# Kernel tuning notes

Hardware: AMD Instinct MI355X
Metric: run time of the kernel (lower is better)

The kernel has to match this reference:

```python
import jax, jax.numpy as jnp
import numpy as np

NUM_HEADS = 8
KEY_DIM = 16
D_V = 32  # attn_ratio * key_dim


def _conv1x1_bn(x, w, s, b):
    # x: [B, Cin, H, W], w: [Cout, Cin]; 1x1 conv == channel contraction,
    # eval-mode BatchNorm folded into per-channel scale s and bias b.
    y = jnp.einsum('bchw,oc->bohw', x, w)
    return y * s[:, None, None] + b[:, None, None]


def setup_inputs() -> dict:
    key = jax.random.key(0)
    ks = jax.random.split(key, 14)
    B, C, H, W = 16, 256, 32, 32
    nh_kd, dh = NUM_HEADS * KEY_DIM, NUM_HEADS * D_V
    f = jax.random.normal
    return {
        'x': f(ks[0], (B, C, H, W), jnp.float32),
        'wq': f(ks[1], (nh_kd, C), jnp.float32) * 0.05,
        'sq': jax.random.uniform(ks[2], (nh_kd,), jnp.float32),
        'bq': f(ks[3], (nh_kd,), jnp.float32) * 0.05,
        'wk': f(ks[4], (nh_kd, C), jnp.float32) * 0.05,
        'sk': jax.random.uniform(ks[5], (nh_kd,), jnp.float32),
        'bk': f(ks[6], (nh_kd,), jnp.float32) * 0.05,
        'wv': f(ks[7], (dh, C), jnp.float32) * 0.05,
        'sv': jax.random.uniform(ks[8], (dh,), jnp.float32),
        'bv': f(ks[9], (dh,), jnp.float32) * 0.05,
        'wp': f(ks[10], (C, dh), jnp.float32) * 0.05,
        'sp': jax.random.uniform(ks[11], (C,), jnp.float32),
        'bp': f(ks[12], (C,), jnp.float32) * 0.05,
    }


def reference(x, wq, sq, bq, wk, sk, bk, wv, sv, bv, wp, sp, bp):
    B, C, H, W = x.shape
    N = H * W
    # QKV projections (1x1 conv + folded BN)
    q = _conv1x1_bn(x, wq, sq, bq).reshape(B, NUM_HEADS, KEY_DIM, N)  # b h k n
    k = _conv1x1_bn(x, wk, sk, bk).reshape(B, NUM_HEADS, KEY_DIM, N)  # b h k m
    v = _conv1x1_bn(x, wv, sv, bv).reshape(B, NUM_HEADS, D_V, N)      # b h d m
    # NOTE: the original forward does NOT apply self.scale to the scores.
    attn = jnp.einsum('bhkn,bhkm->bhnm', q, k)
    attn = jax.nn.softmax(attn, axis=-1)
    out = jnp.einsum('bhnm,bhdm->bhdn', attn, v)  # b h d n
    out = out.reshape(B, NUM_HEADS * D_V, H, W)
    # proj = Sequential(activation, Conv2d_BN): activation FIRST
    out = jax.nn.relu(out)
    return _conv1x1_bn(out, wp, sp, bp)
```

## Files before the change

kernel.cpp:

```cpp
#include <hip/hip_runtime.h>

#define NTOT 1024
#define CIN  256
#define BATCH 16
#define NH   8
#define KD   16
#define DV   32
#define L2E  1.44269504088896340736f

typedef unsigned short u16;
typedef unsigned int   u32;
typedef __attribute__((ext_vector_type(2)))  _Float16 f16x2;
typedef __attribute__((ext_vector_type(8)))  _Float16 f16x8;
typedef __attribute__((ext_vector_type(16))) float    f32x16;

__device__ inline f16x8 as_f16x8(uint4 u) { return __builtin_bit_cast(f16x8, u); }
__device__ inline f16x2 as_f16x2(u32 u)   { return __builtin_bit_cast(f16x2, u); }
__device__ inline u32 pkrtz(float a, float b) {
  return __builtin_bit_cast(u32, __builtin_amdgcn_cvt_pkrtz(a, b));
}
__device__ inline u16 f2h(float x) {
  return __builtin_bit_cast(u16, (_Float16)x);
}
__device__ inline float fexp2(float x) {
#if __has_builtin(__builtin_amdgcn_exp2f)
  return __builtin_amdgcn_exp2f(x);
#else
  float r; asm("v_exp_f32 %0, %1" : "=v"(r) : "v"(x)); return r;
#endif
}
__device__ inline float dot2acc(u32 p2, float c) {
#if __has_builtin(__builtin_amdgcn_fdot2)
  const f16x2 one2 = __builtin_bit_cast(f16x2, (u32)0x3C003C00u);
  return __builtin_amdgcn_fdot2(as_f16x2(p2), one2, c, false);
#else
  const f16x2 v = as_f16x2(p2);
  return c + (float)v[0] + (float)v[1];
#endif
}

__global__ __launch_bounds__(256) void prep_fused(
    const float* __restrict__ X, u16* __restrict__ Xt,
    const float* __restrict__ wq, const float* __restrict__ sq, const float* __restrict__ bq,
    const float* __restrict__ wk, const float* __restrict__ sk, const float* __restrict__ bk,
    const float* __restrict__ wv, const float* __restrict__ sv, const float* __restrict__ bv,
    const float* __restrict__ wp, const float* __restrict__ sp, const float* __restrict__ bp,
    u16* __restrict__ wqkv, u16* __restrict__ wph, float* __restrict__ ball)
{
  __shared__ u16 T[64][64];
  const int bx = blockIdx.x;
  const int t  = threadIdx.x;
  if (bx < 1024) {
    const int n0 = (bx & 15) * 64;
    const int c0 = ((bx >> 4) & 3) * 64;
    const int b  = bx >> 6;
    #pragma unroll
    for (int rr = 0; rr < 4; ++rr) {
      const int c  = rr*16 + (t>>4);
      const int n4 = (t&15)*4;
      const float4 v = *(const float4*)&X[((size_t)b*CIN + c0 + c)*NTOT + n0 + n4];
      ushort4 r; r.x=f2h(v.x); r.y=f2h(v.y); r.z=f2h(v.z); r.w=f2h(v.w);
      *(ushort4*)&T[c][n4] = r;
    }
    __syncthreads();
    const int nl = t & 63;
    #pragma unroll
    for (int j = 0; j < 2; ++j) {
      const int oct = (t>>6)*2 + j;
      uint4 w;
      w.x = (u32)T[oct*8+0][nl] | ((u32)T[oct*8+1][nl] << 16);
      w.y = (u32)T[oct*8+2][nl] | ((u32)T[oct*8+3][nl] << 16);
      w.z = (u32)T[oct*8+4][nl] | ((u32)T[oct*8+5][nl] << 16);
      w.w = (u32)T[oct*8+6][nl] | ((u32)T[oct*8+7][nl] << 16);
      *(uint4*)&Xt[((size_t)b*NTOT + n0 + nl)*CIN + c0 + oct*8] = w;
    }
  } else {
    const int row = (bx - 1024)*4 + (t>>6);
    const int ln  = t & 63;
    const float* src; u16* dst; float sc, bi;
    if (row < 128)      { src = wq + (size_t)row*CIN;       sc = sq[row]*L2E;     bi = bq[row]*L2E;     dst = wqkv + (size_t)row*CIN; }
    else if (row < 256) { src = wk + (size_t)(row-128)*CIN; sc = sk[row-128];     bi = bk[row-128];     dst = wqkv + (size_t)row*CIN; }
    else if (row < 512) { src = wv + (size_t)(row-256)*CIN; sc = sv[row-256];     bi = bv[row-256];     dst = wqkv + (size_t)row*CIN; }
    else                { src = wp + (size_t)(row-512)*CIN; sc = sp[row-512];     bi = bp[row-512];     dst = wph + (size_t)(row-512)*CIN; }
    const float4 v = *(const float4*)&src[ln*4];
    ushort4 r;
    r.x = f2h(v.x*sc); r.y = f2h(v.y*sc); r.z = f2h(v.z*sc); r.w = f2h(v.w*sc);
    *(ushort4*)&dst[ln*4] = r;
    if (ln == 0) ball[row] = bi;
  }
}

template<int BN, int MODE>
__global__ __launch_bounds__(256) void conv_mfma(
    const u16* __restrict__ Wh, const u16* __restrict__ Bt,
    const float* __restrict__ ball,
    u16* __restrict__ q_t, u16* __restrict__ k_t, u16* __restrict__ v_h,
    float* __restrict__ outp)
{
  constexpr int FN = BN / 64;
  constexpr int NB = BN / 32;
  __shared__ u16 A_lds[2][128 * 64];
  __shared__ u16 B_lds[2][BN * 64];
  const int t    = threadIdx.x;
  const int lane = t & 63;
  const int w    = t >> 6;
  const int wm = w >> 1, wn = w & 1;
  const int g = lane >> 5, nl = lane & 31;
  const int n0 = blockIdx.x * BN;
  const int m0 = blockIdx.y * 128;
  const int b  = blockIdx.z;

  f32x16 acc[2][FN] = {};
  uint4 rA[4], rB[NB];

  #pragma unroll
  for (int r = 0; r < 4; ++r) {
    const int idx = t + r*256, row = idx >> 3, ch = idx & 7;
    rA[r] = *(const uint4*)&Wh[(size_t)(m0+row)*CIN + ch*8];
  }
  #pragma unroll
  for (int r = 0; r < NB; ++r) {
    const int idx = t + r*256, row = idx >> 3, ch = idx & 7;
    rB[r] = *(const uint4*)&Bt[((size_t)b*NTOT + n0 + row)*CIN + ch*8];
  }
  #pragma unroll
  for (int r = 0; r < 4; ++r) {
    const int idx = t + r*256, row = idx >> 3, ch = idx & 7;
    *(uint4*)&A_lds[0][row*64 + ((ch ^ (row&7))*8)] = rA[r];
  }
  #pragma unroll
  for (int r = 0; r < NB; ++r) {
    const int idx = t + r*256, row = idx >> 3, ch = idx & 7;
    *(uint4*)&B_lds[0][row*64 + ((ch ^ (row&7))*8)] = rB[r];
  }
  __syncthreads();

  for (int it = 0; it < 4; ++it) {
    const int cur = it & 1;
    if (it < 3) {
      const int c0 = (it+1)*64;
      #pragma unroll
      for (int r = 0; r < 4; ++r) {
        const int idx = t + r*256, row = idx >> 3, ch = idx & 7;
        rA[r] = *(const uint4*)&Wh[(size_t)(m0+row)*CIN + c0 + ch*8];
      }
      #pragma unroll
      for (int r = 0; r < NB; ++r) {
        const int idx = t + r*256, row = idx >> 3, ch = idx & 7;
        rB[r] = *(const uint4*)&Bt[((size_t)b*NTOT + n0 + row)*CIN + c0 + ch*8];
      }
    }
    #pragma unroll
    for (int ks = 0; ks < 4; ++ks) {
      const int ch = 2*ks + g;
      f16x8 a[2], bb[FN];
      #pragma unroll
      for (int fi = 0; fi < 2; ++fi) {
        const int row = wm*64 + fi*32 + nl;
        a[fi] = as_f16x8(*(const uint4*)&A_lds[cur][row*64 + ((ch ^ (row&7))*8)]);
      }
      #pragma unroll
      for (int fj = 0; fj < FN; ++fj) {
        const int row = wn*(BN/2) + fj*32 + nl;
        bb[fj] = as_f16x8(*(const uint4*)&B_lds[cur][row*64 + ((ch ^ (row&7))*8)]);
      }
      #pragma unroll
      for (int fi = 0; fi < 2; ++fi)
        #pragma unroll
        for (int fj = 0; fj < FN; ++fj)
          acc[fi][fj] = __builtin_amdgcn_mfma_f32_32x32x16_f16(a[fi], bb[fj], acc[fi][fj], 0, 0, 0);
    }
    if (it < 3) {
      #pragma unroll
      for (int r = 0; r < 4; ++r) {
        const int idx = t + r*256, row = idx >> 3, ch = idx & 7;
        *(uint4*)&A_lds[cur^1][row*64 + ((ch ^ (row&7))*8)] = rA[r];
      }
      #pragma unroll
      for (int r = 0; r < NB; ++r) {
        const int idx = t + r*256, row = idx >> 3, ch = idx & 7;
        *(uint4*)&B_lds[cur^1][row*64 + ((ch ^ (row&7))*8)] = rB[r];
      }
      __syncthreads();
    }
  }

  #pragma unroll
  for (int fi = 0; fi < 2; ++fi) {
    #pragma unroll
    for (int fj = 0; fj < FN; ++fj) {
      const int n = n0 + wn*(BN/2) + fj*32 + nl;
      #pragma unroll
      for (int q = 0; q < 4; ++q) {
        const int ob = m0 + wm*64 + fi*32 + 8*q + 4*g;
        const float v0 = acc[fi][fj][4*q+0] + ball[ob+0];
        const float v1 = acc[fi][fj][4*q+1] + ball[ob+1];
        const float v2 = acc[fi][fj][4*q+2] + ball[ob+2];
        const float v3 = acc[fi][fj][4*q+3] + ball[ob+3];
        if (MODE == 0) {
          if (ob < 128) {
            const int h = ob >> 4, k0 = ob & 15;
            ushort4 r; r.x = f2h(v0); r.y = f2h(v1); r.z = f2h(v2); r.w = f2h(v3);
            *(ushort4*)&q_t[(((size_t)b*NH + h)*NTOT + n)*KD + k0] = r;
          } else if (ob < 256) {
            const int oo = ob - 128;
            const int h = oo >> 4, k0 = oo & 15;
            const int plane = k0 >> 3, j0 = k0 & 7;
            ushort4 r; r.x = f2h(v0); r.y = f2h(v1); r.z = f2h(v2); r.w = f2h(v3);
            *(ushort4*)&k_t[((((size_t)b*NH + h)*2 + plane)*NTOT + n)*8 + j0] = r;
          } else {
            const int oo = ob - 256;
            const int h = oo >> 5, d0 = oo & 31;
            const int mb = n >> 4, loc = n & 15;
            const int g2 = (loc >> 2) & 1;
            const int j  = (loc & 3) + ((loc >> 3) << 2);
            u16* vp = v_h + (((((size_t)b*NH + h)*64 + mb)*2 + g2)*32 + d0)*8 + j;
            vp[0*8] = f2h(v0);
            vp[1*8] = f2h(v1);
            vp[2*8] = f2h(v2);
            vp[3*8] = f2h(v3);
          }
        } else {
          float* op = outp + ((size_t)b*CIN + ob)*NTOT + n;
          op[0*NTOT] = v0; op[1*NTOT] = v1; op[2*NTOT] = v2; op[3*NTOT] = v3;
        }
      }
    }
  }
}

__global__ __launch_bounds__(1024) void attn_mfma(
    const u16* __restrict__ Qt,
    const u16* __restrict__ Kt,
    const u16* __restrict__ Vt,
    u16* __restrict__ Ot)
{
  __shared__ u16 K_lds[2*NTOT*8];
  __shared__ u16 V_lds[4096*8];
  const int t    = threadIdx.x;
  const int lane = t & 63;
  const int wave = t >> 6;
  const int bh   = blockIdx.x >> 1;
  const int half = blockIdx.x & 1;
  const int g = lane >> 5, nl = lane & 31;
  const int n0 = half*512 + wave*32;

  const u16* Kh = Kt + (size_t)bh*(2*NTOT*8);
  const u16* Vh = Vt + (size_t)bh*(4096*8);
  const u16* Qh = Qt + (size_t)bh*(NTOT*KD);

  #pragma unroll
  for (int r = 0; r < 2; ++r) {
    const int uu = r*1024 + t;
    *(uint4*)&K_lds[uu*8] = *(const uint4*)&Kh[uu*8];
  }
  #pragma unroll
  for (int r = 0; r < 4; ++r) {
    const int uu = r*1024 + t;
    *(uint4*)&V_lds[uu*8] = *(const uint4*)&Vh[uu*8];
  }

  const f16x8 qf = as_f16x8(*(const uint4*)&Qh[(size_t)(n0+nl)*KD + g*8]);
  __syncthreads();

  const f32x16 fzero = {};
  f32x16 acc = {};
  float l0 = 0.f, l1 = 0.f, l2 = 0.f, l3 = 0.f;
  const char* Kb = (const char*)K_lds + g*16384 + nl*16;
  const char* Vb = (const char*)V_lds + g*512   + nl*16;

  f16x8 kf  = as_f16x8(*(const uint4*)(Kb));
  uint4 va0 = *(const uint4*)(Vb);
  uint4 va1 = *(const uint4*)(Vb + 1024);
  f32x16 s_cur = __builtin_amdgcn_mfma_f32_32x32x16_f16(kf, qf, fzero, 0, 0, 0);

  #pragma unroll 2
  for (int st = 0; st < 31; ++st) {
    const f16x8 kfn = as_f16x8(*(const uint4*)(Kb + (st+1)*512));
    __builtin_amdgcn_s_setprio(1);
    const f32x16 s_next = __builtin_amdgcn_mfma_f32_32x32x16_f16(kfn, qf, fzero, 0, 0, 0);
    __builtin_amdgcn_s_setprio(0);
    const uint4 nva0 = *(const uint4*)(Vb + (st+1)*2048);
    const uint4 nva1 = *(const uint4*)(Vb + (st+1)*2048 + 1024);

    {
      float p[8];
      #pragma unroll
      for (int r = 0; r < 8; ++r) p[r] = fexp2(s_cur[r]);
      uint4 pb0;
      pb0.x = pkrtz(p[0], p[1]); pb0.y = pkrtz(p[2], p[3]);
      pb0.z = pkrtz(p[4], p[5]); pb0.w = pkrtz(p[6], p[7]);
      l0 = dot2acc(pb0.x, l0); l1 = dot2acc(pb0.y, l1);
      l2 = dot2acc(pb0.z, l2); l3 = dot2acc(pb0.w, l3);
      __builtin_amdgcn_s_setprio(1);
      acc = __builtin_amdgcn_mfma_f32_32x32x16_f16(as_f16x8(va0), as_f16x8(pb0), acc, 0, 0, 0);
      __builtin_amdgcn_s_setprio(0);
    }
    {
      float p[8];
      #pragma unroll
      for (int r = 0; r < 8; ++r) p[r] = fexp2(s_cur[8+r]);
      uint4 pb1;
      pb1.x = pkrtz(p[0], p[1]); pb1.y = pkrtz(p[2], p[3]);
      pb1.z = pkrtz(p[4], p[5]); pb1.w = pkrtz(p[6], p[7]);
      l0 = dot2acc(pb1.x, l0); l1 = dot2acc(pb1.y, l1);
      l2 = dot2acc(pb1.z, l2); l3 = dot2acc(pb1.w, l3);
      __builtin_amdgcn_s_setprio(1);
      acc = __builtin_amdgcn_mfma_f32_32x32x16_f16(as_f16x8(va1), as_f16x8(pb1), acc, 0, 0, 0);
      __builtin_amdgcn_s_setprio(0);
    }
    s_cur = s_next; va0 = nva0; va1 = nva1;
  }
  {
    {
      float p[8];
      #pragma unroll
      for (int r = 0; r < 8; ++r) p[r] = fexp2(s_cur[r]);
      uint4 pb0;
      pb0.x = pkrtz(p[0], p[1]); pb0.y = pkrtz(p[2], p[3]);
      pb0.z = pkrtz(p[4], p[5]); pb0.w = pkrtz(p[6], p[7]);
      l0 = dot2acc(pb0.x, l0); l1 = dot2acc(pb0.y, l1);
      l2 = dot2acc(pb0.z, l2); l3 = dot2acc(pb0.w, l3);
      acc = __builtin_amdgcn_mfma_f32_32x32x16_f16(as_f16x8(va0), as_f16x8(pb0), acc, 0, 0, 0);
    }
    {
      float p[8];
      #pragma unroll
      for (int r = 0; r < 8; ++r) p[r] = fexp2(s_cur[8+r]);
      uint4 pb1;
      pb1.x = pkrtz(p[0], p[1]); pb1.y = pkrtz(p[2], p[3]);
      pb1.z = pkrtz(p[4], p[5]); pb1.w = pkrtz(p[6], p[7]);
      l0 = dot2acc(pb1.x, l0); l1 = dot2acc(pb1.y, l1);
      l2 = dot2acc(pb1.z, l2); l3 = dot2acc(pb1.w, l3);
      acc = __builtin_amdgcn_mfma_f32_32x32x16_f16(as_f16x8(va1), as_f16x8(pb1), acc, 0, 0, 0);
    }
  }

  const float lp = (l0 + l1) + (l2 + l3);
  const float lt = lp + __shfl_xor(lp, 32);
  const float rl = 1.0f / lt;
  const int b = bh >> 3, h = bh & 7;
  u16* op = Ot + ((size_t)b*NTOT + n0 + nl)*CIN + h*DV;
  #pragma unroll
  for (int q = 0; q < 4; ++q) {
    const float v0 = fmaxf(acc[4*q+0]*rl, 0.f);
    const float v1 = fmaxf(acc[4*q+1]*rl, 0.f);
    const float v2 = fmaxf(acc[4*q+2]*rl, 0.f);
    const float v3 = fmaxf(acc[4*q+3]*rl, 0.f);
    uint2 pk; pk.x = pkrtz(v0, v1); pk.y = pkrtz(v2, v3);
    *(uint2*)&op[8*q + 4*g] = pk;
  }
}

extern "C" void kernel_launch(void* const* d_in, const int* in_sizes, int n_in,
                              void* d_out, int out_size, void* d_ws, size_t ws_size,
                              hipStream_t stream) {
  const float* x  = (const float*)d_in[0];
  const float* wq = (const float*)d_in[1];
  const float* sq = (const float*)d_in[2];
  const float* bq = (const float*)d_in[3];
  const float* wk = (const float*)d_in[4];
  const float* sk = (const float*)d_in[5];
  const float* bk = (const float*)d_in[6];
  const float* wv = (const float*)d_in[7];
  const float* sv = (const float*)d_in[8];
  const float* bv = (const float*)d_in[9];
  const float* wp = (const float*)d_in[10];
  const float* sp = (const float*)d_in[11];
  const float* bp = (const float*)d_in[12];
  float* out = (float*)d_out;

  char* ws = (char*)d_ws;
  u16*   x_t  = (u16*)(ws);
  u16*   q_t  = (u16*)(ws + (8u  << 20));
  u16*   k_t  = (u16*)(ws + (12u << 20));
  u16*   v_h  = (u16*)(ws + (16u << 20));
  u16*   wqkv = (u16*)(ws + (24u << 20));
  u16*   wph  = (u16*)(ws + (24u << 20) + (256u << 10));
  float* ball = (float*)(ws + (24u << 20) + (384u << 10));

  prep_fused<<<dim3(1216), dim3(256), 0, stream>>>(
      x, x_t, wq, sq, bq, wk, sk, bk, wv, sv, bv, wp, sp, bp, wqkv, wph, ball);
  conv_mfma<128, 0><<<dim3(8, 4, 16), dim3(256), 0, stream>>>(
      wqkv, x_t, ball, q_t, k_t, v_h, nullptr);
  attn_mfma<<<dim3(256), dim3(1024), 0, stream>>>(q_t, k_t, v_h, x_t );
  conv_mfma<64, 1><<<dim3(16, 2, 16), dim3(256), 0, stream>>>(
      wph, x_t , ball + 512, nullptr, nullptr, nullptr, out);
}
```

Before: 57.36 us.

## Fuse all four stages into one cooperative kernel with grid syncs

Replaces the four separate launches (prep, QKV conv, attention, projection conv) with a single cooperative persistent kernel of 256 blocks x 1024 threads. The stages are separated by grid.sync, and each stage's tiling is re-mapped onto the fixed block count. This removes inter-kernel launch gaps and tail effects, at the cost of grid-barrier overhead and conv stages that now run at only one block per CU with different tile shapes. If the cooperative launch fails, it falls back to the old four-kernel path.

```diff
diff --git a/kernel.cpp b/kernel.cpp
--- a/kernel.cpp
+++ b/kernel.cpp
@@ -1,4 +1,7 @@
 #include <hip/hip_runtime.h>
+#include <hip/hip_cooperative_groups.h>
+
+namespace cg = cooperative_groups;
 
 #define NTOT 1024
 #define CIN  256
@@ -37,6 +40,291 @@
   const f16x2 v = as_f16x2(p2);
   return c + (float)v[0] + (float)v[1];
 #endif
+}
+
+__global__ __launch_bounds__(1024) void mega(
+    const float* __restrict__ X,
+    const float* __restrict__ wq, const float* __restrict__ sq, const float* __restrict__ bq,
+    const float* __restrict__ wk, const float* __restrict__ sk, const float* __restrict__ bk,
+    const float* __restrict__ wv, const float* __restrict__ sv, const float* __restrict__ bv,
+    const float* __restrict__ wp, const float* __restrict__ sp, const float* __restrict__ bp,
+    u16* __restrict__ x_t,
+    u16* __restrict__ q_t, u16* __restrict__ k_t, u16* __restrict__ v_h,
+    u16* __restrict__ wqkv, u16* __restrict__ wph, float* __restrict__ ball,
+    float* __restrict__ out)
+{
+  __shared__ __align__(16) char SMEM[98304];
+  cg::grid_group grid = cg::this_grid();
+  const int t    = threadIdx.x;
+  const int bid  = blockIdx.x;
+  const int lane = t & 63;
+  const int w    = t >> 6;
+  const int g = lane >> 5, nl = lane & 31;
+
+  {
+    const int q4 = t >> 8, tt = t & 255;
+    const int ti = bid*4 + q4;
+    const int n0 = (ti & 15)*64, c0 = ((ti >> 4) & 3)*64, b = ti >> 6;
+    u16 (*T)[64] = (u16(*)[64])(SMEM + q4*8192);
+    #pragma unroll
+    for (int rr = 0; rr < 4; ++rr) {
+      const int c  = rr*16 + (tt >> 4);
+      const int n4 = (tt & 15)*4;
+      const float4 v = *(const float4*)&X[((size_t)b*CIN + c0 + c)*NTOT + n0 + n4];
+      ushort4 r; r.x = f2h(v.x); r.y = f2h(v.y); r.z = f2h(v.z); r.w = f2h(v.w);
+      *(ushort4*)&T[c][n4] = r;
+    }
+    __syncthreads();
+    const int nl2 = tt & 63;
+    #pragma unroll
+    for (int j = 0; j < 2; ++j) {
+      const int oct = (tt >> 6)*2 + j;
+      uint4 wv4;
+      wv4.x = (u32)T[oct*8+0][nl2] | ((u32)T[oct*8+1][nl2] << 16);
+      wv4.y = (u32)T[oct*8+2][nl2] | ((u32)T[oct*8+3][nl2] << 16);
+      wv4.z = (u32)T[oct*8+4][nl2] | ((u32)T[oct*8+5][nl2] << 16);
+      wv4.w = (u32)T[oct*8+6][nl2] | ((u32)T[oct*8+7][nl2] << 16);
+      *(uint4*)&x_t[((size_t)b*NTOT + n0 + nl2)*CIN + c0 + oct*8] = wv4;
+    }
+    if (bid < 48) {
+      const int row = bid*16 + (t >> 6);
+      const int ln  = t & 63;
+      const float* src; u16* dst; float sc, bi;
+      if (row < 128)      { src = wq + (size_t)row*CIN;       sc = sq[row]*L2E;     bi = bq[row]*L2E;     dst = wqkv + (size_t)row*CIN; }
+      else if (row < 256) { src = wk + (size_t)(row-128)*CIN; sc = sk[row-128];     bi = bk[row-128];     dst = wqkv + (size_t)row*CIN; }
+      else if (row < 512) { src = wv + (size_t)(row-256)*CIN; sc = sv[row-256];     bi = bv[row-256];     dst = wqkv + (size_t)row*CIN; }
+      else                { src = wp + (size_t)(row-512)*CIN; sc = sp[row-512];     bi = bp[row-512];     dst = wph + (size_t)(row-512)*CIN; }
+      const float4 v = *(const float4*)&src[ln*4];
+      ushort4 r;
+      r.x = f2h(v.x*sc); r.y = f2h(v.y*sc); r.z = f2h(v.z*sc); r.w = f2h(v.w*sc);
+      *(ushort4*)&dst[ln*4] = r;
+      if (ln == 0) ball[row] = bi;
+    }
+  }
+  grid.sync();
+
+  {
+    u16* A_lds = (u16*)SMEM;
+    u16* B_lds = (u16*)(SMEM + 16384);
+    const int wm = w >> 3, wn = w & 7;
+    const int np = bid & 3, mp = (bid >> 2) & 3, b = bid >> 4;
+    const int n0 = np*256, m0 = mp*128;
+    f32x16 acc[2] = {};
+
+    for (int c0 = 0; c0 < CIN; c0 += 64) {
+      { const int row = t >> 3, ch = t & 7;
+        *(uint4*)&A_lds[row*64 + ((ch ^ (row&7))*8)] =
+            *(const uint4*)&wqkv[(size_t)(m0+row)*CIN + c0 + ch*8]; }
+      #pragma unroll
+      for (int r = 0; r < 2; ++r) {
+        const int idx = t + r*1024, row = idx >> 3, ch = idx & 7;
+        *(uint4*)&B_lds[row*64 + ((ch ^ (row&7))*8)] =
+            *(const uint4*)&x_t[((size_t)b*NTOT + n0 + row)*CIN + c0 + ch*8];
+      }
+      __syncthreads();
+      #pragma unroll
+      for (int ks = 0; ks < 4; ++ks) {
+        const int ch = 2*ks + g;
+        const int ra0 = wm*64 + nl, ra1 = wm*64 + 32 + nl, rb = wn*32 + nl;
+        const f16x8 a0 = as_f16x8(*(const uint4*)&A_lds[ra0*64 + ((ch ^ (ra0&7))*8)]);
+        const f16x8 a1 = as_f16x8(*(const uint4*)&A_lds[ra1*64 + ((ch ^ (ra1&7))*8)]);
+        const f16x8 bb = as_f16x8(*(const uint4*)&B_lds[rb*64 + ((ch ^ (rb&7))*8)]);
+        acc[0] = __builtin_amdgcn_mfma_f32_32x32x16_f16(a0, bb, acc[0], 0, 0, 0);
+        acc[1] = __builtin_amdgcn_mfma_f32_32x32x16_f16(a1, bb, acc[1], 0, 0, 0);
+      }
+      __syncthreads();
+    }
+
+    const int n = n0 + wn*32 + nl;
+    #pragma unroll
+    for (int fi = 0; fi < 2; ++fi) {
+      #pragma unroll
+      for (int q = 0; q < 4; ++q) {
+        const int ob = m0 + wm*64 + fi*32 + 8*q + 4*g;
+        const float v0 = acc[fi][4*q+0] + ball[ob+0];
+        const float v1 = acc[fi][4*q+1] + ball[ob+1];
+        const float v2 = acc[fi][4*q+2] + ball[ob+2];
+        const float v3 = acc[fi][4*q+3] + ball[ob+3];
+        if (ob < 128) {
+          const int h = ob >> 4, k0 = ob & 15;
+          ushort4 r; r.x = f2h(v0); r.y = f2h(v1); r.z = f2h(v2); r.w = f2h(v3);
+          *(ushort4*)&q_t[(((size_t)b*NH + h)*NTOT + n)*KD + k0] = r;
+        } else if (ob < 256) {
+          const int oo = ob - 128;
+          const int h = oo >> 4, k0 = oo & 15;
+          const int plane = k0 >> 3, j0 = k0 & 7;
+          ushort4 r; r.x = f2h(v0); r.y = f2h(v1); r.z = f2h(v2); r.w = f2h(v3);
+          *(ushort4*)&k_t[((((size_t)b*NH + h)*2 + plane)*NTOT + n)*8 + j0] = r;
+        } else {
+          const int oo = ob - 256;
+          const int h = oo >> 5, d0 = oo & 31;
+          const int mb = n >> 4, loc = n & 15;
+          const int g2 = (loc >> 2) & 1;
+          const int j  = (loc & 3) + ((loc >> 3) << 2);
+          u16* vp = v_h + (((((size_t)b*NH + h)*64 + mb)*2 + g2)*32 + d0)*8 + j;
+          vp[0*8] = f2h(v0);
+          vp[1*8] = f2h(v1);
+          vp[2*8] = f2h(v2);
+          vp[3*8] = f2h(v3);
+        }
+      }
+    }
+  }
+  grid.sync();
+
+  {
+    u16* K_lds = (u16*)SMEM;
+    u16* V_lds = (u16*)(SMEM + 32768);
+    const int bh = bid >> 1, half = bid & 1;
+    const int n0 = half*512 + w*32;
+
+    const u16* Kh = k_t + (size_t)bh*(2*NTOT*8);
+    const u16* Vh = v_h + (size_t)bh*(4096*8);
+    const u16* Qh = q_t + (size_t)bh*(NTOT*KD);
+
+    #pragma unroll
+    for (int r = 0; r < 2; ++r) {
+      const int uu = r*1024 + t;
+      *(uint4*)&K_lds[uu*8] = *(const uint4*)&Kh[uu*8];
+    }
+    #pragma unroll
+    for (int r = 0; r < 4; ++r) {
+      const int uu = r*1024 + t;
+      *(uint4*)&V_lds[uu*8] = *(const uint4*)&Vh[uu*8];
+    }
+
+    const f16x8 qf = as_f16x8(*(const uint4*)&Qh[(size_t)(n0+nl)*KD + g*8]);
+    __syncthreads();
+
+    const f32x16 fzero = {};
+    f32x16 acc = {};
+    float l0 = 0.f, l1 = 0.f, l2 = 0.f, l3 = 0.f;
+    const char* Kb = (const char*)K_lds + g*16384 + nl*16;
+    const char* Vb = (const char*)V_lds + g*512   + nl*16;
+
+    f16x8 kf  = as_f16x8(*(const uint4*)(Kb));
+    uint4 va0 = *(const uint4*)(Vb);
+    uint4 va1 = *(const uint4*)(Vb + 1024);
+    f32x16 s_cur = __builtin_amdgcn_mfma_f32_32x32x16_f16(kf, qf, fzero, 0, 0, 0);
+
+    #pragma unroll 2
+    for (int st = 0; st < 31; ++st) {
+      const f16x8 kfn = as_f16x8(*(const uint4*)(Kb + (st+1)*512));
+      __builtin_amdgcn_s_setprio(1);
+      const f32x16 s_next = __builtin_amdgcn_mfma_f32_32x32x16_f16(kfn, qf, fzero, 0, 0, 0);
+      __builtin_amdgcn_s_setprio(0);
+      const uint4 nva0 = *(const uint4*)(Vb + (st+1)*2048);
+      const uint4 nva1 = *(const uint4*)(Vb + (st+1)*2048 + 1024);
+
+      {
+        float p[8];
+        #pragma unroll
+        for (int r = 0; r < 8; ++r) p[r] = fexp2(s_cur[r]);
+        uint4 pb0;
+        pb0.x = pkrtz(p[0], p[1]); pb0.y = pkrtz(p[2], p[3]);
+        pb0.z = pkrtz(p[4], p[5]); pb0.w = pkrtz(p[6], p[7]);
+        l0 = dot2acc(pb0.x, l0); l1 = dot2acc(pb0.y, l1);
+        l2 = dot2acc(pb0.z, l2); l3 = dot2acc(pb0.w, l3);
+        __builtin_amdgcn_s_setprio(1);
+        acc = __builtin_amdgcn_mfma_f32_32x32x16_f16(as_f16x8(va0), as_f16x8(pb0), acc, 0, 0, 0);
+        __builtin_amdgcn_s_setprio(0);
+      }
+      {
+        float p[8];
+        #pragma unroll
+        for (int r = 0; r < 8; ++r) p[r] = fexp2(s_cur[8+r]);
+        uint4 pb1;
+        pb1.x = pkrtz(p[0], p[1]); pb1.y = pkrtz(p[2], p[3]);
+        pb1.z = pkrtz(p[4], p[5]); pb1.w = pkrtz(p[6], p[7]);
+        l0 = dot2acc(pb1.x, l0); l1 = dot2acc(pb1.y, l1);
+        l2 = dot2acc(pb1.z, l2); l3 = dot2acc(pb1.w, l3);
+        __builtin_amdgcn_s_setprio(1);
+        acc = __builtin_amdgcn_mfma_f32_32x32x16_f16(as_f16x8(va1), as_f16x8(pb1), acc, 0, 0, 0);
+        __builtin_amdgcn_s_setprio(0);
+      }
+      s_cur = s_next; va0 = nva0; va1 = nva1;
+    }
+    {
+      {
+        float p[8];
+        #pragma unroll
+        for (int r = 0; r < 8; ++r) p[r] = fexp2(s_cur[r]);
+        uint4 pb0;
+        pb0.x = pkrtz(p[0], p[1]); pb0.y = pkrtz(p[2], p[3]);
+        pb0.z = pkrtz(p[4], p[5]); pb0.w = pkrtz(p[6], p[7]);
+        l0 = dot2acc(pb0.x, l0); l1 = dot2acc(pb0.y, l1);
+        l2 = dot2acc(pb0.z, l2); l3 = dot2acc(pb0.w, l3);
+        acc = __builtin_amdgcn_mfma_f32_32x32x16_f16(as_f16x8(va0), as_f16x8(pb0), acc, 0, 0, 0);
+      }
+      {
+        float p[8];
+        #pragma unroll
+        for (int r = 0; r < 8; ++r) p[r] = fexp2(s_cur[8+r]);
+        uint4 pb1;
+        pb1.x = pkrtz(p[0], p[1]); pb1.y = pkrtz(p[2], p[3]);
+        pb1.z = pkrtz(p[4], p[5]); pb1.w = pkrtz(p[6], p[7]);
+        l0 = dot2acc(pb1.x, l0); l1 = dot2acc(pb1.y, l1);
+        l2 = dot2acc(pb1.z, l2); l3 = dot2acc(pb1.w, l3);
+        acc = __builtin_amdgcn_mfma_f32_32x32x16_f16(as_f16x8(va1), as_f16x8(pb1), acc, 0, 0, 0);
+      }
+    }
+
+    const float lp = (l0 + l1) + (l2 + l3);
+    const float lt = lp + __shfl_xor(lp, 32);
+    const float rl = 1.0f / lt;
+    const int b = bh >> 3, h = bh & 7;
+    u16* op = x_t  + ((size_t)b*NTOT + n0 + nl)*CIN + h*DV;
+    #pragma unroll
+    for (int q = 0; q < 4; ++q) {
+      const float v0 = fmaxf(acc[4*q+0]*rl, 0.f);
+      const float v1 = fmaxf(acc[4*q+1]*rl, 0.f);
+      const float v2 = fmaxf(acc[4*q+2]*rl, 0.f);
+      const float v3 = fmaxf(acc[4*q+3]*rl, 0.f);
+      uint2 pk; pk.x = pkrtz(v0, v1); pk.y = pkrtz(v2, v3);
+      *(uint2*)&op[8*q + 4*g] = pk;
+    }
+  }
+  grid.sync();
+
+  {
+    u16* A_lds = (u16*)SMEM;
+    u16* B_lds = (u16*)(SMEM + 16384);
+    const int wm = w >> 2, wn = w & 3;
+    const int np = bid & 7, mp = (bid >> 3) & 1, b = bid >> 4;
+    const int n0 = np*128, m0 = mp*128;
+    const float* ball2 = ball + 512;
+    f32x16 acc = {};
+
+    for (int c0 = 0; c0 < CIN; c0 += 64) {
+      { const int row = t >> 3, ch = t & 7;
+        *(uint4*)&A_lds[row*64 + ((ch ^ (row&7))*8)] =
+            *(const uint4*)&wph[(size_t)(m0+row)*CIN + c0 + ch*8]; }
+      { const int row = t >> 3, ch = t & 7;
+        *(uint4*)&B_lds[row*64 + ((ch ^ (row&7))*8)] =
+            *(const uint4*)&x_t[((size_t)b*NTOT + n0 + row)*CIN + c0 + ch*8]; }
+      __syncthreads();
+      #pragma unroll
+      for (int ks = 0; ks < 4; ++ks) {
+        const int ch = 2*ks + g;
+        const int ra = wm*32 + nl, rb = wn*32 + nl;
+        const f16x8 a  = as_f16x8(*(const uint4*)&A_lds[ra*64 + ((ch ^ (ra&7))*8)]);
+        const f16x8 bb = as_f16x8(*(const uint4*)&B_lds[rb*64 + ((ch ^ (rb&7))*8)]);
+        acc = __builtin_amdgcn_mfma_f32_32x32x16_f16(a, bb, acc, 0, 0, 0);
+      }
+      __syncthreads();
+    }
+
+    const int n = n0 + wn*32 + nl;
+    #pragma unroll
+    for (int q = 0; q < 4; ++q) {
+      const int ob = m0 + wm*32 + 8*q + 4*g;
+      float* op = out + ((size_t)b*CIN + ob)*NTOT + n;
+      op[0*NTOT] = acc[4*q+0] + ball2[ob+0];
+      op[1*NTOT] = acc[4*q+1] + ball2[ob+1];
+      op[2*NTOT] = acc[4*q+2] + ball2[ob+2];
+      op[3*NTOT] = acc[4*q+3] + ball2[ob+3];
+    }
+  }
 }
 
 __global__ __launch_bounds__(256) void prep_fused(
@@ -67,12 +355,12 @@
     #pragma unroll
     for (int j = 0; j < 2; ++j) {
       const int oct = (t>>6)*2 + j;
-      uint4 w;
-      w.x = (u32)T[oct*8+0][nl] | ((u32)T[oct*8+1][nl] << 16);
-      w.y = (u32)T[oct*8+2][nl] | ((u32)T[oct*8+3][nl] << 16);
-      w.z = (u32)T[oct*8+4][nl] | ((u32)T[oct*8+5][nl] << 16);
-      w.w = (u32)T[oct*8+6][nl] | ((u32)T[oct*8+7][nl] << 16);
-      *(uint4*)&Xt[((size_t)b*NTOT + n0 + nl)*CIN + c0 + oct*8] = w;
+      uint4 wv4;
+      wv4.x = (u32)T[oct*8+0][nl] | ((u32)T[oct*8+1][nl] << 16);
+      wv4.y = (u32)T[oct*8+2][nl] | ((u32)T[oct*8+3][nl] << 16);
+      wv4.z = (u32)T[oct*8+4][nl] | ((u32)T[oct*8+5][nl] << 16);
+      wv4.w = (u32)T[oct*8+6][nl] | ((u32)T[oct*8+7][nl] << 16);
+      *(uint4*)&Xt[((size_t)b*NTOT + n0 + nl)*CIN + c0 + oct*8] = wv4;
     }
   } else {
     const int row = (bx - 1024)*4 + (t>>6);
@@ -230,10 +518,8 @@
 }
 
 __global__ __launch_bounds__(1024) void attn_mfma(
-    const u16* __restrict__ Qt,
-    const u16* __restrict__ Kt,
-    const u16* __restrict__ Vt,
-    u16* __restrict__ Ot)
+    const u16* __restrict__ Qt, const u16* __restrict__ Kt,
+    const u16* __restrict__ Vt, u16* __restrict__ Ot)
 {
   __shared__ u16 K_lds[2*NTOT*8];
   __shared__ u16 V_lds[4096*8];
@@ -282,7 +568,6 @@
     __builtin_amdgcn_s_setprio(0);
     const uint4 nva0 = *(const uint4*)(Vb + (st+1)*2048);
     const uint4 nva1 = *(const uint4*)(Vb + (st+1)*2048 + 1024);
-
     {
       float p[8];
       #pragma unroll
@@ -379,11 +664,24 @@
   u16*   wph  = (u16*)(ws + (24u << 20) + (256u << 10));
   float* ball = (float*)(ws + (24u << 20) + (384u << 10));
 
-  prep_fused<<<dim3(1216), dim3(256), 0, stream>>>(
-      x, x_t, wq, sq, bq, wk, sk, bk, wv, sv, bv, wp, sp, bp, wqkv, wph, ball);
-  conv_mfma<128, 0><<<dim3(8, 4, 16), dim3(256), 0, stream>>>(
-      wqkv, x_t, ball, q_t, k_t, v_h, nullptr);
-  attn_mfma<<<dim3(256), dim3(1024), 0, stream>>>(q_t, k_t, v_h, x_t );
-  conv_mfma<64, 1><<<dim3(16, 2, 16), dim3(256), 0, stream>>>(
-      wph, x_t , ball + 512, nullptr, nullptr, nullptr, out);
-}
+  void* ka[] = { (void*)&x,
+                 (void*)&wq, (void*)&sq, (void*)&bq,
+                 (void*)&wk, (void*)&sk, (void*)&bk,
+                 (void*)&wv, (void*)&sv, (void*)&bv,
+                 (void*)&wp, (void*)&sp, (void*)&bp,
+                 (void*)&x_t, (void*)&q_t, (void*)&k_t, (void*)&v_h,
+                 (void*)&wqkv, (void*)&wph, (void*)&ball, (void*)&out };
+  hipError_t err = hipLaunchCooperativeKernel(
+      (void*)mega, dim3(256), dim3(1024), ka, 0, stream);
+
+  if (err != hipSuccess) {
+    (void)hipGetLastError();
+    prep_fused<<<dim3(1216), dim3(256), 0, stream>>>(
+        x, x_t, wq, sq, bq, wk, sk, bk, wv, sv, bv, wp, sp, bp, wqkv, wph, ball);
+    conv_mfma<128, 0><<<dim3(8, 4, 16), dim3(256), 0, stream>>>(
+        wqkv, x_t, ball, q_t, k_t, v_h, nullptr);
+    attn_mfma<<<dim3(256), dim3(1024), 0, stream>>>(q_t, k_t, v_h, x_t);
+    conv_mfma<64, 1><<<dim3(16, 2, 16), dim3(256), 0, stream>>>(
+        wph, x_t, ball + 512, nullptr, nullptr, nullptr, out);
+  }
+}
```

Result: slower. 181.2 us (+215.9%).
